# Performance work log

Measured on AMD Instinct MI355X. Metric: run time of the kernel, lower is better.

The kernel has to match this reference:

```python
import jax, jax.numpy as jnp
import numpy as np

N = 240000
B = 2
GRID = (480, 360, 32)
NUM_CLASS = 20
IGNORE_LABEL = 0
MINB = np.array([0.0, -np.pi, -4.0], np.float32)
MAXB = np.array([50.0, np.pi, 2.0], np.float32)
EPS = 1e-5


def setup_inputs() -> dict:
    key = jax.random.key(0)
    ks = jax.random.split(key, 32)
    d = {}
    d['pt_fea'] = jax.random.normal(ks[0], (N, 6), jnp.float32)
    # cylindrical coords (rho, phi, z) uniformly inside the volume
    u = jax.random.uniform(ks[1], (N, 3), jnp.float32)
    d['xyz'] = u * jnp.asarray(MAXB - MINB) + jnp.asarray(MINB)
    d['batch_idx'] = jnp.sort(jax.random.randint(ks[2], (N,), 0, B)).astype(jnp.int64)
    d['pt_lab'] = jax.random.randint(ks[3], (N,), 0, NUM_CLASS).astype(jnp.int64)
    d['shuffled_ind'] = jnp.arange(N, dtype=jnp.int64)  # identity perm (deterministic)
    i = 4
    for name, c in [('bn0', 9), ('bn1', 64), ('bn2', 128), ('bn3', 256)]:
        d[name + '_g'] = jax.random.uniform(ks[i], (c,), jnp.float32, 0.5, 1.5); i += 1
        d[name + '_b'] = jax.random.normal(ks[i], (c,), jnp.float32) * 0.1; i += 1
        d[name + '_m'] = jax.random.normal(ks[i], (c,), jnp.float32) * 0.1; i += 1
        d[name + '_v'] = jax.random.uniform(ks[i], (c,), jnp.float32, 0.5, 1.5); i += 1
    for name, (fi, fo) in [('1', (9, 64)), ('2', (64, 128)), ('3', (128, 256)), ('4', (256, 256))]:
        d['w' + name] = jax.random.normal(ks[i], (fi, fo), jnp.float32) / np.sqrt(fi); i += 1
        d['b' + name] = jax.random.normal(ks[i], (fo,), jnp.float32) * 0.01; i += 1
    d['wc'] = jax.random.normal(ks[i], (256, 16), jnp.float32) / 16.0; i += 1
    d['bc'] = jax.random.normal(ks[i], (16,), jnp.float32) * 0.01
    return d


def _bn(x, g, b, m, v):
    return (x - m) * (g * jax.lax.rsqrt(v + EPS)) + b


def _ppmodel(feat, bn0_g, bn0_b, bn0_m, bn0_v, w1, b1, bn1_g, bn1_b, bn1_m, bn1_v,
             w2, b2, bn2_g, bn2_b, bn2_m, bn2_v, w3, b3, bn3_g, bn3_b, bn3_m, bn3_v, w4, b4):
    x = _bn(feat, bn0_g, bn0_b, bn0_m, bn0_v)
    x = jax.nn.relu(_bn(x @ w1 + b1, bn1_g, bn1_b, bn1_m, bn1_v))
    x = jax.nn.relu(_bn(x @ w2 + b2, bn2_g, bn2_b, bn2_m, bn2_v))
    x = jax.nn.relu(_bn(x @ w3 + b3, bn3_g, bn3_b, bn3_m, bn3_v))
    return x @ w4 + b4  # [N, 256]


def reference(pt_fea, xyz, batch_idx, pt_lab, shuffled_ind,
              bn0_g, bn0_b, bn0_m, bn0_v, w1, b1, bn1_g, bn1_b, bn1_m, bn1_v,
              w2, b2, bn2_g, bn2_b, bn2_m, bn2_v, w3, b3, bn3_g, bn3_b, bn3_m, bn3_v,
              w4, b4, wc, bc):
    minb = jnp.asarray(MINB)
    maxb = jnp.asarray(MAXB)
    grid = jnp.asarray(np.array(GRID, np.float32))
    intervals = (maxb - minb) / (grid - 1.0)

    clamped = jnp.clip(xyz, minb, maxb)
    ind = jnp.floor((clamped - minb) / intervals).astype(jnp.int32)  # [N,3]
    voxel_centers = (ind.astype(jnp.float32) + 0.5) * intervals + minb
    rel_xyz = xyz - voxel_centers
    feat = jnp.concatenate([rel_xyz, pt_fea], axis=1)  # [N,9]

    bi = batch_idx.astype(jnp.int32)
    counts = jnp.full((B,) + GRID + (NUM_CLASS,), IGNORE_LABEL, jnp.int32)
    counts = counts.at[bi, ind[:, 0], ind[:, 1], ind[:, 2], pt_lab].add(1)
    voxel_labels = jnp.argmax(counts, axis=-1).astype(jnp.int32)  # [B,480,360,32]

    feat = feat[shuffled_ind]

    flat = ((bi.astype(jnp.int64) * GRID[0] + ind[:, 0]) * GRID[1] + ind[:, 1]) * GRID[2] + ind[:, 2]
    unq, unq_inv = jnp.unique(flat, size=N, fill_value=-1, return_inverse=True)
    unq_inv = unq_inv.reshape(-1)

    processed = _ppmodel(feat, bn0_g, bn0_b, bn0_m, bn0_v, w1, b1, bn1_g, bn1_b, bn1_m, bn1_v,
                         w2, b2, bn2_g, bn2_b, bn2_m, bn2_v, w3, b3, bn3_g, bn3_b, bn3_m, bn3_v, w4, b4)
    pooled = jax.ops.segment_max(processed, unq_inv, num_segments=N)
    seg_cnt = jax.ops.segment_sum(jnp.ones((N,), jnp.float32), unq_inv, num_segments=N)
    pooled = jnp.where(seg_cnt[:, None] > 0, pooled, 0.0)  # zero out empty (padded) segments

    processed_pooled = jax.nn.relu(pooled @ wc + bc)  # fea_compression

    cat_pt_ind = jnp.concatenate([batch_idx[:, None], ind.astype(jnp.int64)], axis=1)
    return (unq, processed_pooled, voxel_labels, cat_pt_ind)
```

## Files before the change

kernel.cpp:

```cpp
#include <hip/hip_runtime.h>
#include <stdint.h>

#define N_PTS 240000
#define NV    11059200
#define NWORDS 172800
#define NB_PT 938
#define NB_WORD 675
#define NBLK_MLP 3750
#define PA 264

typedef __bf16 bf16x8 __attribute__((ext_vector_type(8)));
typedef short  short8 __attribute__((ext_vector_type(8)));
typedef float  f32x4  __attribute__((ext_vector_type(4)));

__device__ __forceinline__ unsigned short f2bf(float f) {
  unsigned u = __builtin_bit_cast(unsigned, f);
  return (unsigned short)((u + 0x7FFFu + ((u >> 16) & 1u)) >> 16);
}
__device__ __forceinline__ float bf2f(unsigned short h) {
  unsigned u = ((unsigned)h) << 16;
  return __builtin_bit_cast(float, u);
}

__device__ __forceinline__ unsigned block_sum(unsigned v, unsigned* s4, int t) {
  #pragma unroll
  for (int o = 32; o; o >>= 1) v += __shfl_down(v, o);
  if ((t & 63) == 0) s4[t >> 6] = v;
  __syncthreads();
  unsigned r = s4[0] + s4[1] + s4[2] + s4[3];
  __syncthreads();
  return r;
}

__global__ void prep_vox_kernel(
    const float* __restrict__ bng0, const float* __restrict__ bnb0, const float* __restrict__ bnm0, const float* __restrict__ bnv0,
    const float* __restrict__ bng1, const float* __restrict__ bnb1, const float* __restrict__ bnm1, const float* __restrict__ bnv1,
    const float* __restrict__ bng2, const float* __restrict__ bnb2, const float* __restrict__ bnm2, const float* __restrict__ bnv2,
    const float* __restrict__ bng3, const float* __restrict__ bnb3, const float* __restrict__ bnm3, const float* __restrict__ bnv3,
    const float* __restrict__ w1, const float* __restrict__ b1,
    const float* __restrict__ w2, const float* __restrict__ b2,
    const float* __restrict__ w3, const float* __restrict__ b3,
    const float* __restrict__ w4, const float* __restrict__ wc,
    float* __restrict__ s0, float* __restrict__ t0, float* __restrict__ w1e, float* __restrict__ be1,
    float* __restrict__ be2, float* __restrict__ be3,
    unsigned short* __restrict__ w2t, unsigned short* __restrict__ w3t, unsigned short* __restrict__ w4t,
    unsigned short* __restrict__ wct,
    const float* __restrict__ xyz, const int* __restrict__ bidx,
    unsigned* __restrict__ flatkeys, unsigned long long* __restrict__ bitmap,
    float* __restrict__ out_cat, float* __restrict__ out_unq)
{
  if (blockIdx.x < 256) {
    const int id = blockIdx.x * 256 + threadIdx.x;
    { int c = id >> 8, k = id & 255; w4t[c * 256 + k] = f2bf(w4[k * 256 + c]); }
    if (id < 32768) { int c = id >> 7, k = id & 127;
      float s = bng3[c] * rsqrtf(bnv3[c] + 1e-5f);
      w3t[c * 128 + k] = f2bf(w3[k * 256 + c] * s); }
    if (id < 8192) { int c = id >> 6, k = id & 63;
      float s = bng2[c] * rsqrtf(bnv2[c] + 1e-5f);
      w2t[c * 64 + k] = f2bf(w2[k * 128 + c] * s); }
    if (id < 4096) { int c = id >> 8, k = id & 255;
      wct[c * 256 + k] = f2bf(wc[k * 16 + c]); }
    if (id < 576) { int k = id / 64, c = id % 64;
      float s = bng1[c] * rsqrtf(bnv1[c] + 1e-5f);
      w1e[k * 64 + c] = w1[k * 64 + c] * s; }
    if (id < 64)  { float s = bng1[id] * rsqrtf(bnv1[id] + 1e-5f); be1[id] = (b1[id] - bnm1[id]) * s + bnb1[id]; }
    if (id < 128) { float s = bng2[id] * rsqrtf(bnv2[id] + 1e-5f); be2[id] = (b2[id] - bnm2[id]) * s + bnb2[id]; }
    if (id < 256) { float s = bng3[id] * rsqrtf(bnv3[id] + 1e-5f); be3[id] = (b3[id] - bnm3[id]) * s + bnb3[id]; }
    if (id < 9)   { float s = bng0[id] * rsqrtf(bnv0[id] + 1e-5f); s0[id] = s; t0[id] = bnb0[id] - bnm0[id] * s; }
    return;
  }
  const int j = (blockIdx.x - 256) * 256 + threadIdx.x;
  if (j >= N_PTS) return;
  out_unq[j] = -1.0f;
  const float PI_F = 3.14159265358979323846f;
  const float minb[3] = {0.0f, -PI_F, -4.0f};
  const float maxb[3] = {50.0f, PI_F, 2.0f};
  const float gm1[3]  = {479.0f, 359.0f, 31.0f};
  int ind[3];
  #pragma unroll
  for (int d = 0; d < 3; ++d) {
    float itv = (maxb[d] - minb[d]) / gm1[d];
    float x  = xyz[(size_t)j * 3 + d];
    float cl = fminf(fmaxf(x, minb[d]), maxb[d]);
    ind[d] = (int)floorf((cl - minb[d]) / itv);
  }
  const int bi = bidx[j];
  const unsigned flat = ((unsigned)(bi * 480 + ind[0]) * 360u + (unsigned)ind[1]) * 32u + (unsigned)ind[2];
  flatkeys[j] = flat;
  atomicOr(&bitmap[flat >> 6], 1ull << (flat & 63u));
  float* oc = out_cat + (size_t)j * 4;
  oc[0] = (float)bi; oc[1] = (float)ind[0]; oc[2] = (float)ind[1]; oc[3] = (float)ind[2];
}

__global__ void reduce_words(const unsigned long long* __restrict__ bm, unsigned* __restrict__ bsums) {
  __shared__ unsigned sh[256];
  const int w = blockIdx.x * 256 + threadIdx.x;
  sh[threadIdx.x] = (unsigned)__popcll(bm[w]);
  __syncthreads();
  for (int s = 128; s > 0; s >>= 1) { if (threadIdx.x < s) sh[threadIdx.x] += sh[threadIdx.x + s]; __syncthreads(); }
  if (threadIdx.x == 0) bsums[blockIdx.x] = sh[0];
}

__global__ __launch_bounds__(256) void scatter_unq(
    const unsigned long long* __restrict__ bm, const unsigned* __restrict__ bsums,
    unsigned* __restrict__ wordpref, unsigned* __restrict__ unqvals, float* __restrict__ out_unq)
{
  __shared__ unsigned sh[256];
  __shared__ unsigned s4[4];
  const int t = threadIdx.x, b = blockIdx.x;
  const int w = b * 256 + t;
  unsigned long long word = bm[w];
  unsigned own = (unsigned)__popcll(word);
  sh[t] = own; __syncthreads();
  for (int off = 1; off < 256; off <<= 1) {
    unsigned v = (t >= off) ? sh[t - off] : 0u;
    __syncthreads(); sh[t] += v; __syncthreads();
  }
  unsigned v = 0;
  for (int i = t; i < b; i += 256) v += bsums[i];
  const unsigned excl = block_sum(v, s4, t);
  unsigned r = excl + sh[t] - own;
  wordpref[w] = r;
  while (word) {
    int bit = __builtin_ctzll(word);
    unsigned id = (unsigned)w * 64u + (unsigned)bit;
    unqvals[r] = id;
    out_unq[r] = (float)id;
    ++r;
    word &= word - 1;
  }
}

__global__ void inv_kernel(const unsigned* __restrict__ flatkeys, const unsigned long long* __restrict__ bm,
                           const unsigned* __restrict__ wordpref,
                           unsigned* __restrict__ unq_inv, unsigned* __restrict__ cnt) {
  const int j = blockIdx.x * 256 + threadIdx.x;
  if (j >= N_PTS) return;
  const unsigned f = flatkeys[j];
  const unsigned w = f >> 6, b = f & 63u;
  const unsigned r = wordpref[w] + (unsigned)__popcll(bm[w] & ((1ull << b) - 1ull));
  unq_inv[j] = r;
  atomicAdd(&cnt[r], 1u);
}

__global__ void reduce_cnt(const unsigned* __restrict__ cnt, unsigned* __restrict__ bsums) {
  __shared__ unsigned sh[256];
  const int j = blockIdx.x * 256 + threadIdx.x;
  sh[threadIdx.x] = (j < N_PTS) ? cnt[j] : 0u;
  __syncthreads();
  for (int s = 128; s > 0; s >>= 1) { if (threadIdx.x < s) sh[threadIdx.x] += sh[threadIdx.x + s]; __syncthreads(); }
  if (threadIdx.x == 0) bsums[blockIdx.x] = sh[0];
}

__global__ __launch_bounds__(256) void scan_cnt(
    const unsigned* __restrict__ cnt, const unsigned* __restrict__ bsums,
    unsigned* __restrict__ off, unsigned* __restrict__ cur)
{
  __shared__ unsigned sh[256];
  __shared__ unsigned s4[4];
  const int t = threadIdx.x, b = blockIdx.x;
  const int j = b * 256 + t;
  unsigned own = (j < N_PTS) ? cnt[j] : 0u;
  sh[t] = own; __syncthreads();
  for (int o = 1; o < 256; o <<= 1) {
    unsigned v = (t >= o) ? sh[t - o] : 0u;
    __syncthreads(); sh[t] += v; __syncthreads();
  }
  unsigned v = 0;
  for (int i = t; i < b; i += 256) v += bsums[i];
  const unsigned excl = block_sum(v, s4, t);
  if (j < N_PTS) { unsigned e = excl + sh[t] - own; off[j] = e; cur[j] = e; }
}

__global__ void plist_fill_kernel(const unsigned* __restrict__ unq_inv, unsigned* __restrict__ cur,
                                  unsigned long long* __restrict__ plist64,
                                  const unsigned* __restrict__ cnt, const float* __restrict__ bc,
                                  float* __restrict__ out_pooled) {
  const int j = blockIdx.x * 256 + threadIdx.x;
  if (j >= N_PTS) return;
  const unsigned r = unq_inv[j];
  plist64[atomicAdd(&cur[r], 1u)] = ((unsigned long long)r << 32) | (unsigned)j;
  if (cnt[j] == 0) {
    #pragma unroll
    for (int c = 0; c < 16; ++c) out_pooled[(size_t)j * 16 + c] = fmaxf(bc[c], 0.f);
  }
}

template<int K, int C, bool RELU, bool MIDB>
__device__ __forceinline__ void gemm_stage(
    const unsigned short* __restrict__ Wt,
    const float* __restrict__ bias,
    const unsigned short* in,
    unsigned short* outp,
    int wave, int l15, int quad)
{
  constexpr int KC = K / 32;
  constexpr int NT = C / 128;
  f32x4 acc[4][NT];
  #pragma unroll
  for (int mt = 0; mt < 4; ++mt)
    #pragma unroll
    for (int nt = 0; nt < NT; ++nt) acc[mt][nt] = (f32x4){0.f, 0.f, 0.f, 0.f};
  const unsigned short* wp[NT];
  #pragma unroll
  for (int nt = 0; nt < NT; ++nt)
    wp[nt] = Wt + (size_t)(wave * 16 * NT + nt * 16 + l15) * K + quad * 8;
  #pragma unroll
  for (int kc = 0; kc < KC; ++kc) {
    bf16x8 b[NT];
    #pragma unroll
    for (int nt = 0; nt < NT; ++nt)
      b[nt] = __builtin_bit_cast(bf16x8, *(const short8*)(wp[nt] + kc * 32));
    #pragma unroll
    for (int mt = 0; mt < 4; ++mt) {
      bf16x8 a = __builtin_bit_cast(bf16x8, *(const short8*)&in[(mt * 16 + l15) * PA + kc * 32 + quad * 8]);
      #pragma unroll
      for (int nt = 0; nt < NT; ++nt)
        acc[mt][nt] = __builtin_amdgcn_mfma_f32_16x16x32_bf16(b[nt], a, acc[mt][nt], 0, 0, 0);
    }
  }
  if (MIDB) __syncthreads();
  #pragma unroll
  for (int mt = 0; mt < 4; ++mt)
    #pragma unroll
    for (int nt = 0; nt < NT; ++nt) {
      const int cbase = wave * 16 * NT + nt * 16 + quad * 4;
      const f32x4 bs = *(const f32x4*)&bias[cbase];
      unsigned short h[4];
      #pragma unroll
      for (int r = 0; r < 4; ++r) {
        float y = acc[mt][nt][r] + bs[r];
        if (RELU) y = fmaxf(y, 0.f);
        h[r] = f2bf(y);
      }
      uint2 pk; pk.x = (unsigned)h[0] | ((unsigned)h[1] << 16);
      pk.y = (unsigned)h[2] | ((unsigned)h[3] << 16);
      *(uint2*)&outp[(mt * 16 + l15) * PA + cbase] = pk;
    }
  __syncthreads();
}

__global__ __launch_bounds__(512, 8) void mlp_pool_kernel(
    const float* __restrict__ ptfea, const float* __restrict__ xyz, const int* __restrict__ shuf,
    const unsigned long long* __restrict__ plist64,
    const unsigned* __restrict__ offv, const unsigned* __restrict__ cnt,
    const int* __restrict__ ptlab, const unsigned* __restrict__ unqvals,
    const float* __restrict__ s0, const float* __restrict__ t0,
    const float* __restrict__ w1e, const float* __restrict__ be1,
    const unsigned short* __restrict__ w2t, const float* __restrict__ be2,
    const unsigned short* __restrict__ w3t, const float* __restrict__ be3,
    const unsigned short* __restrict__ w4t, const float* __restrict__ b4,
    const unsigned short* __restrict__ wct, const float* __restrict__ bc,
    unsigned short* __restrict__ partials, float* __restrict__ out_pooled,
    float* __restrict__ out_lab)
{
  __shared__ __align__(16) unsigned short buf[64 * PA];
  __shared__ int segs[64];
  __shared__ int jrows[64];
  __shared__ int s_alast;
  __shared__ int s_nrun;
  __shared__ unsigned short s_runs[32];
  __shared__ unsigned char s_lead[64], s_comp[64];
  const int tid  = threadIdx.x;
  const int wave = tid >> 6, lane = tid & 63;
  const int l15 = lane & 15, quad = lane >> 4;
  const int row0 = blockIdx.x * 64;

  if (tid == 0) { s_alast = 0; s_nrun = 0; }
  if (tid < 64) {
    const unsigned long long v = plist64[row0 + tid];
    jrows[tid] = (int)(unsigned)v;
    segs[tid]  = (int)(unsigned)(v >> 32);
  }

  {
    const int r = tid >> 3, part = tid & 7;
    const int sj = shuf[(unsigned)plist64[row0 + r]];
    const float PI_F = 3.14159265358979323846f;
    const float minb[3] = {0.0f, -PI_F, -4.0f};
    const float maxb[3] = {50.0f, PI_F, 2.0f};
    const float gm1[3]  = {479.0f, 359.0f, 31.0f};
    float x0[9];
    #pragma unroll
    for (int d = 0; d < 3; ++d) {
      float itv = (maxb[d] - minb[d]) / gm1[d];
      float x   = xyz[(size_t)sj * 3 + d];
      float cl  = fminf(fmaxf(x, minb[d]), maxb[d]);
      float fi  = floorf((cl - minb[d]) / itv);
      float center = (fi + 0.5f) * itv + minb[d];
      x0[d] = (x - center) * s0[d] + t0[d];
    }
    #pragma unroll
    for (int d = 0; d < 6; ++d) x0[3 + d] = ptfea[(size_t)sj * 6 + d] * s0[3 + d] + t0[3 + d];
    unsigned short h[8];
    #pragma unroll
    for (int ci = 0; ci < 8; ++ci) {
      float acc = be1[part * 8 + ci];
      #pragma unroll
      for (int k = 0; k < 9; ++k) acc += x0[k] * w1e[k * 64 + part * 8 + ci];
      h[ci] = f2bf(fmaxf(acc, 0.0f));
    }
    *(short8*)&buf[r * PA + part * 8] = *(short8*)&h[0];
  }
  __syncthreads();

  if (tid < 64) {
    const int r = tid;
    bool lead = (r == 0) || (segs[r] != segs[r - 1]);
    s_lead[r] = lead ? 1 : 0;
    unsigned char comp = 0;
    int e = r + 1;
    if (lead) {
      atomicMax(&s_alast, r);
      while (e < 64 && segs[e] == segs[r]) ++e;
      const unsigned s = (unsigned)segs[r];
      comp = (offv[s] == (unsigned)(row0 + r) && offv[s] + cnt[s] == (unsigned)(row0 + e)) ? 1 : 0;
    }
    s_comp[r] = comp;
    if (comp) {
      int bestl;
      if (e - r == 1) bestl = ptlab[jrows[r]];
      else {
        int bestc = 0; bestl = 32;
        for (int i = r; i < e; ++i) {
          const int li = ptlab[jrows[i]];
          int cc = 0;
          for (int k2 = r; k2 < e; ++k2) cc += (ptlab[jrows[k2]] == li) ? 1 : 0;
          if (cc > bestc || (cc == bestc && li < bestl)) { bestc = cc; bestl = li; }
        }
      }
      out_lab[unqvals[segs[r]]] = (float)bestl;
    }
    const bool multi = lead && (e - r) > 1;
    unsigned long long mm = __ballot(multi);
    if (multi) {
      int idx = (int)__popcll(mm & ((1ull << r) - 1ull));
      s_runs[idx] = (unsigned short)((r << 8) | e);
    }
    if (tid == 0) s_nrun = (int)__popcll(mm);
  }

  gemm_stage< 64, 128, true,  false>(w2t, be2, buf,       buf + 136, wave, l15, quad);
  gemm_stage<128, 256, true,  true >(w3t, be3, buf + 136, buf,       wave, l15, quad);
  gemm_stage<256, 256, false, true >(w4t, b4,  buf,       buf,       wave, l15, quad);

  if (tid < 256) {
    const int n = s_nrun;
    for (int i = 0; i < n; ++i) {
      const int re = s_runs[i];
      const int r = re >> 8, e = re & 255;
      float m = bf2f(buf[r * PA + tid]);
      for (int rr = r + 1; rr < e; ++rr) m = fmaxf(m, bf2f(buf[rr * PA + tid]));
      buf[r * PA + tid] = f2bf(m);
    }
  }
  __syncthreads();

  if (tid < 256) {
    const int c = tid;
    const int alast = s_alast;
    const size_t b2 = (size_t)blockIdx.x * 2;
    if (!s_comp[0])     partials[b2 * 256 + c]       = buf[0 * PA + c];
    if (!s_comp[alast]) partials[(b2 + 1) * 256 + c] = buf[alast * PA + c];
  }

  if (wave < 4) {
    const unsigned short* wp = wct + l15 * 256 + quad * 8;
    f32x4 acc = (f32x4){0.f, 0.f, 0.f, 0.f};
    #pragma unroll
    for (int kc = 0; kc < 8; ++kc) {
      bf16x8 w = __builtin_bit_cast(bf16x8, *(const short8*)(wp + kc * 32));
      bf16x8 x = __builtin_bit_cast(bf16x8, *(const short8*)&buf[(wave * 16 + l15) * PA + kc * 32 + quad * 8]);
      acc = __builtin_amdgcn_mfma_f32_16x16x32_bf16(w, x, acc, 0, 0, 0);
    }
    const int r1 = wave * 16 + l15;
    if (s_lead[r1] && s_comp[r1]) {
      const f32x4 bcv = *(const f32x4*)&bc[quad * 4];
      f32x4 v;
      #pragma unroll
      for (int r = 0; r < 4; ++r) v[r] = fmaxf(acc[r] + bcv[r], 0.f);
      *(f32x4*)&out_pooled[(size_t)segs[r1] * 16 + quad * 4] = v;
    }
  }
}

__global__ __launch_bounds__(256) void merge_kernel(
    const unsigned long long* __restrict__ plist64,
    const unsigned* __restrict__ offv, const unsigned* __restrict__ cnt,
    const unsigned short* __restrict__ partials,
    const int* __restrict__ ptlab, const unsigned* __restrict__ unqvals,
    const float* __restrict__ wc, const float* __restrict__ bc,
    float* __restrict__ out_pooled, float* __restrict__ out_lab)
{
  __shared__ float pooled[256];
  __shared__ float psum[256];
  const int b = blockIdx.x;
  const unsigned s = (unsigned)(plist64[(size_t)b * 64 + 63] >> 32);
  const unsigned o = offv[s], e = o + cnt[s];
  if ((o >> 6) != (unsigned)b) return;
  if (e <= (unsigned)(b + 1) * 64) return;
  const int B1 = (int)((e - 1) >> 6);
  const int c = threadIdx.x;
  float m = bf2f(partials[((size_t)2 * b + 1) * 256 + c]);
  for (int bb = b + 1; bb <= B1; ++bb)
    m = fmaxf(m, bf2f(partials[(size_t)2 * bb * 256 + c]));
  pooled[c] = m;
  __syncthreads();
  const int co = c & 15, kg = c >> 4;
  float p = 0.f;
  #pragma unroll
  for (int k = kg * 16; k < kg * 16 + 16; ++k) p += pooled[k] * wc[k * 16 + co];
  psum[c] = p;
  __syncthreads();
  if (c < 16) {
    float acc = bc[c];
    #pragma unroll
    for (int g = 0; g < 16; ++g) acc += psum[g * 16 + c];
    out_pooled[(size_t)s * 16 + c] = fmaxf(acc, 0.f);
  }
  if (c == 0) {
    int bestc = 0, bestl = 32;
    for (unsigned i = o; i < e; ++i) {
      const int li = ptlab[(unsigned)plist64[i]];
      int cc = 0;
      for (unsigned k2 = o; k2 < e; ++k2) cc += (ptlab[(unsigned)plist64[k2]] == li) ? 1 : 0;
      if (cc > bestc || (cc == bestc && li < bestl)) { bestc = cc; bestl = li; }
    }
    out_lab[unqvals[s]] = (float)bestl;
  }
}

extern "C" void kernel_launch(void* const* d_in, const int* in_sizes, int n_in,
                              void* d_out, int out_size, void* d_ws, size_t ws_size,
                              hipStream_t stream)
{
  const float* pt_fea = (const float*)d_in[0];
  const float* xyz    = (const float*)d_in[1];
  const int*   bidx   = (const int*)d_in[2];
  const int*   ptlab  = (const int*)d_in[3];
  const int*   shuf   = (const int*)d_in[4];
  const float* bng0 = (const float*)d_in[5],  *bnb0 = (const float*)d_in[6],  *bnm0 = (const float*)d_in[7],  *bnv0 = (const float*)d_in[8];
  const float* bng1 = (const float*)d_in[9],  *bnb1 = (const float*)d_in[10], *bnm1 = (const float*)d_in[11], *bnv1 = (const float*)d_in[12];
  const float* bng2 = (const float*)d_in[13], *bnb2 = (const float*)d_in[14], *bnm2 = (const float*)d_in[15], *bnv2 = (const float*)d_in[16];
  const float* bng3 = (const float*)d_in[17], *bnb3 = (const float*)d_in[18], *bnm3 = (const float*)d_in[19], *bnv3 = (const float*)d_in[20];
  const float* w1 = (const float*)d_in[21], *b1 = (const float*)d_in[22];
  const float* w2 = (const float*)d_in[23], *b2 = (const float*)d_in[24];
  const float* w3 = (const float*)d_in[25], *b3 = (const float*)d_in[26];
  const float* w4 = (const float*)d_in[27], *b4 = (const float*)d_in[28];
  const float* wc = (const float*)d_in[29], *bc = (const float*)d_in[30];

  float* out        = (float*)d_out;
  float* out_unq    = out;
  float* out_pooled = out + 240000;
  float* out_lab    = out + 4080000;
  float* out_cat    = out + 15139200;

  char* wsb = (char*)d_ws;
  size_t o = 0;
  auto alloc = [&](size_t bytes) -> void* { void* p = wsb + o; o = (o + bytes + 255) & ~(size_t)255; return p; };
  unsigned long long* bitmap = (unsigned long long*)alloc((size_t)NWORDS * 8);
  unsigned* cnt    = (unsigned*)alloc((size_t)N_PTS * 4);
  const size_t zero_bytes = o;
  float* s0  = (float*)alloc(9 * 4);
  float* t0  = (float*)alloc(9 * 4);
  float* w1e = (float*)alloc(576 * 4);
  float* be1 = (float*)alloc(64 * 4);
  float* be2 = (float*)alloc(128 * 4);
  float* be3 = (float*)alloc(256 * 4);
  unsigned short* w2t = (unsigned short*)alloc(8192 * 2);
  unsigned short* w3t = (unsigned short*)alloc(32768 * 2);
  unsigned short* w4t = (unsigned short*)alloc(65536 * 2);
  unsigned short* wct = (unsigned short*)alloc(4096 * 2);
  unsigned* flatkeys = (unsigned*)alloc((size_t)N_PTS * 4);
  unsigned* unq_inv  = (unsigned*)alloc((size_t)N_PTS * 4);
  unsigned* unqvals  = (unsigned*)alloc((size_t)N_PTS * 4);
  unsigned* offv     = (unsigned*)alloc((size_t)N_PTS * 4);
  unsigned* cur      = (unsigned*)alloc((size_t)N_PTS * 4);
  unsigned long long* plist64 = (unsigned long long*)alloc((size_t)N_PTS * 8);
  unsigned* wordpref = (unsigned*)alloc((size_t)NWORDS * 4);
  unsigned* bsumA    = (unsigned*)alloc(NB_WORD * 4);
  unsigned* bsumB    = (unsigned*)alloc(NB_PT * 4);
  unsigned short* partials = (unsigned short*)alloc((size_t)NBLK_MLP * 2 * 256 * 2);

  hipMemsetAsync(bitmap, 0, zero_bytes, stream);
  hipMemsetAsync(out_lab, 0, (size_t)NV * 4, stream);

  prep_vox_kernel<<<256 + NB_PT, 256, 0, stream>>>(
      bng0, bnb0, bnm0, bnv0, bng1, bnb1, bnm1, bnv1,
      bng2, bnb2, bnm2, bnv2, bng3, bnb3, bnm3, bnv3,
      w1, b1, w2, b2, w3, b3, w4, wc,
      s0, t0, w1e, be1, be2, be3, w2t, w3t, w4t, wct,
      xyz, bidx, flatkeys, bitmap, out_cat, out_unq);
  reduce_words<<<NB_WORD, 256, 0, stream>>>(bitmap, bsumA);
  scatter_unq<<<NB_WORD, 256, 0, stream>>>(bitmap, bsumA, wordpref, unqvals, out_unq);
  inv_kernel<<<NB_PT, 256, 0, stream>>>(flatkeys, bitmap, wordpref, unq_inv, cnt);
  reduce_cnt<<<NB_PT, 256, 0, stream>>>(cnt, bsumB);
  scan_cnt<<<NB_PT, 256, 0, stream>>>(cnt, bsumB, offv, cur);
  plist_fill_kernel<<<NB_PT, 256, 0, stream>>>(unq_inv, cur, plist64, cnt, bc, out_pooled);
  mlp_pool_kernel<<<NBLK_MLP, 512, 0, stream>>>(pt_fea, xyz, shuf, plist64, offv, cnt,
                                                ptlab, unqvals,
                                                s0, t0, w1e, be1, w2t, be2, w3t, be3, w4t, b4,
                                                wct, bc, partials, out_pooled, out_lab);
  merge_kernel<<<NBLK_MLP, 256, 0, stream>>>(plist64, offv, cnt, partials,
                                             ptlab, unqvals, wc, bc, out_pooled, out_lab);
}
```

Baseline: 402.4 us.

## Process two 64-row windows per block to reuse weight fragments; fuse zeroing into prep

The MLP/pool kernel now runs 256-thread blocks that each handle two 64-point windows. Every wave loads a weight fragment once and applies it to both windows' activations, so global weight traffic per point is halved. The cost is twice the LDS per block and more accumulator registers (launch bounds 256,2), which lowers occupancy. The separate memset of the label volume and of cnt is also folded into the prep kernel as a grid-stride zeroing loop, removing one memset launch.

```diff
diff --git a/kernel.cpp b/kernel.cpp
--- a/kernel.cpp
+++ b/kernel.cpp
@@ -6,7 +6,8 @@
 #define NWORDS 172800
 #define NB_PT 938
 #define NB_WORD 675
-#define NBLK_MLP 3750
+#define NWIN   3750
+#define NBLK_MLP 1875
 #define PA 264
 
 typedef __bf16 bf16x8 __attribute__((ext_vector_type(8)));
@@ -47,10 +48,15 @@
     unsigned short* __restrict__ wct,
     const float* __restrict__ xyz, const int* __restrict__ bidx,
     unsigned* __restrict__ flatkeys, unsigned long long* __restrict__ bitmap,
-    float* __restrict__ out_cat, float* __restrict__ out_unq)
-{
+    unsigned* __restrict__ cnt,
+    float* __restrict__ out_cat, float* __restrict__ out_unq, float* __restrict__ out_lab)
+{
+  const int gtid = blockIdx.x * 256 + threadIdx.x;
+  for (unsigned i = (unsigned)gtid; i < NV / 4; i += (256 + NB_PT) * 256)
+    *(f32x4*)&out_lab[(size_t)i * 4] = (f32x4){0.f, 0.f, 0.f, 0.f};
+  if (gtid < N_PTS) cnt[gtid] = 0u;
   if (blockIdx.x < 256) {
-    const int id = blockIdx.x * 256 + threadIdx.x;
+    const int id = gtid;
     { int c = id >> 8, k = id & 255; w4t[c * 256 + k] = f2bf(w4[k * 256 + c]); }
     if (id < 32768) { int c = id >> 7, k = id & 127;
       float s = bng3[c] * rsqrtf(bnv3[c] + 1e-5f);
@@ -187,20 +193,20 @@
 }
 
 template<int K, int C, bool RELU, bool MIDB>
-__device__ __forceinline__ void gemm_stage(
+__device__ __forceinline__ void gemm_stage2(
     const unsigned short* __restrict__ Wt,
     const float* __restrict__ bias,
-    const unsigned short* in,
-    unsigned short* outp,
+    const unsigned short* inA, unsigned short* outA,
+    const unsigned short* inB, unsigned short* outB,
     int wave, int l15, int quad)
 {
   constexpr int KC = K / 32;
-  constexpr int NT = C / 128;
-  f32x4 acc[4][NT];
+  constexpr int NT = C / 64;
+  f32x4 accA[4][NT], accB[4][NT];
   #pragma unroll
   for (int mt = 0; mt < 4; ++mt)
     #pragma unroll
-    for (int nt = 0; nt < NT; ++nt) acc[mt][nt] = (f32x4){0.f, 0.f, 0.f, 0.f};
+    for (int nt = 0; nt < NT; ++nt) { accA[mt][nt] = (f32x4){0.f,0.f,0.f,0.f}; accB[mt][nt] = (f32x4){0.f,0.f,0.f,0.f}; }
   const unsigned short* wp[NT];
   #pragma unroll
   for (int nt = 0; nt < NT; ++nt)
@@ -213,10 +219,13 @@
       b[nt] = __builtin_bit_cast(bf16x8, *(const short8*)(wp[nt] + kc * 32));
     #pragma unroll
     for (int mt = 0; mt < 4; ++mt) {
-      bf16x8 a = __builtin_bit_cast(bf16x8, *(const short8*)&in[(mt * 16 + l15) * PA + kc * 32 + quad * 8]);
+      bf16x8 aA = __builtin_bit_cast(bf16x8, *(const short8*)&inA[(mt * 16 + l15) * PA + kc * 32 + quad * 8]);
+      bf16x8 aB = __builtin_bit_cast(bf16x8, *(const short8*)&inB[(mt * 16 + l15) * PA + kc * 32 + quad * 8]);
       #pragma unroll
-      for (int nt = 0; nt < NT; ++nt)
-        acc[mt][nt] = __builtin_amdgcn_mfma_f32_16x16x32_bf16(b[nt], a, acc[mt][nt], 0, 0, 0);
+      for (int nt = 0; nt < NT; ++nt) {
+        accA[mt][nt] = __builtin_amdgcn_mfma_f32_16x16x32_bf16(b[nt], aA, accA[mt][nt], 0, 0, 0);
+        accB[mt][nt] = __builtin_amdgcn_mfma_f32_16x16x32_bf16(b[nt], aB, accB[mt][nt], 0, 0, 0);
+      }
     }
   }
   if (MIDB) __syncthreads();
@@ -226,21 +235,23 @@
     for (int nt = 0; nt < NT; ++nt) {
       const int cbase = wave * 16 * NT + nt * 16 + quad * 4;
       const f32x4 bs = *(const f32x4*)&bias[cbase];
-      unsigned short h[4];
+      unsigned short hA[4], hB[4];
       #pragma unroll
       for (int r = 0; r < 4; ++r) {
-        float y = acc[mt][nt][r] + bs[r];
-        if (RELU) y = fmaxf(y, 0.f);
-        h[r] = f2bf(y);
+        float yA = accA[mt][nt][r] + bs[r];
+        float yB = accB[mt][nt][r] + bs[r];
+        if (RELU) { yA = fmaxf(yA, 0.f); yB = fmaxf(yB, 0.f); }
+        hA[r] = f2bf(yA); hB[r] = f2bf(yB);
       }
-      uint2 pk; pk.x = (unsigned)h[0] | ((unsigned)h[1] << 16);
-      pk.y = (unsigned)h[2] | ((unsigned)h[3] << 16);
-      *(uint2*)&outp[(mt * 16 + l15) * PA + cbase] = pk;
-    }
-  __syncthreads();
-}
-
-__global__ __launch_bounds__(512, 8) void mlp_pool_kernel(
+      uint2 pkA; pkA.x = (unsigned)hA[0] | ((unsigned)hA[1] << 16); pkA.y = (unsigned)hA[2] | ((unsigned)hA[3] << 16);
+      uint2 pkB; pkB.x = (unsigned)hB[0] | ((unsigned)hB[1] << 16); pkB.y = (unsigned)hB[2] | ((unsigned)hB[3] << 16);
+      *(uint2*)&outA[(mt * 16 + l15) * PA + cbase] = pkA;
+      *(uint2*)&outB[(mt * 16 + l15) * PA + cbase] = pkB;
+    }
+  __syncthreads();
+}
+
+__global__ __launch_bounds__(256, 2) void mlp_pool_kernel(
     const float* __restrict__ ptfea, const float* __restrict__ xyz, const int* __restrict__ shuf,
     const unsigned long long* __restrict__ plist64,
     const unsigned* __restrict__ offv, const unsigned* __restrict__ cnt,
@@ -254,28 +265,31 @@
     unsigned short* __restrict__ partials, float* __restrict__ out_pooled,
     float* __restrict__ out_lab)
 {
-  __shared__ __align__(16) unsigned short buf[64 * PA];
-  __shared__ int segs[64];
-  __shared__ int jrows[64];
-  __shared__ int s_alast;
-  __shared__ int s_nrun;
-  __shared__ unsigned short s_runs[32];
-  __shared__ unsigned char s_lead[64], s_comp[64];
+  __shared__ __align__(16) unsigned short bufA[64 * PA];
+  __shared__ __align__(16) unsigned short bufB[64 * PA];
+  __shared__ int segs[128];
+  __shared__ int jrows[128];
+  __shared__ int s_alast[2];
+  __shared__ int s_nrun[2];
+  __shared__ unsigned short s_runs[2][32];
+  __shared__ unsigned char s_lead[128], s_comp[128];
   const int tid  = threadIdx.x;
   const int wave = tid >> 6, lane = tid & 63;
   const int l15 = lane & 15, quad = lane >> 4;
-  const int row0 = blockIdx.x * 64;
-
-  if (tid == 0) { s_alast = 0; s_nrun = 0; }
-  if (tid < 64) {
-    const unsigned long long v = plist64[row0 + tid];
+  const int rowbase = blockIdx.x * 128;
+
+  if (tid < 2) { s_alast[tid] = 0; s_nrun[tid] = 0; }
+  if (tid < 128) {
+    const unsigned long long v = plist64[rowbase + tid];
     jrows[tid] = (int)(unsigned)v;
     segs[tid]  = (int)(unsigned)(v >> 32);
   }
 
-  {
-    const int r = tid >> 3, part = tid & 7;
-    const int sj = shuf[(unsigned)plist64[row0 + r]];
+  #pragma unroll
+  for (int w = 0; w < 2; ++w) {
+    const int rl = tid >> 2, part = tid & 3;
+    const int sj = shuf[(unsigned)plist64[rowbase + w * 64 + rl]];
+    unsigned short* bf = w ? bufB : bufA;
     const float PI_F = 3.14159265358979323846f;
     const float minb[3] = {0.0f, -PI_F, -4.0f};
     const float maxb[3] = {50.0f, PI_F, 2.0f};
@@ -292,94 +306,102 @@
     }
     #pragma unroll
     for (int d = 0; d < 6; ++d) x0[3 + d] = ptfea[(size_t)sj * 6 + d] * s0[3 + d] + t0[3 + d];
-    unsigned short h[8];
-    #pragma unroll
-    for (int ci = 0; ci < 8; ++ci) {
-      float acc = be1[part * 8 + ci];
+    unsigned short h[16];
+    #pragma unroll
+    for (int ci = 0; ci < 16; ++ci) {
+      float acc = be1[part * 16 + ci];
       #pragma unroll
-      for (int k = 0; k < 9; ++k) acc += x0[k] * w1e[k * 64 + part * 8 + ci];
+      for (int k = 0; k < 9; ++k) acc += x0[k] * w1e[k * 64 + part * 16 + ci];
       h[ci] = f2bf(fmaxf(acc, 0.0f));
     }
-    *(short8*)&buf[r * PA + part * 8] = *(short8*)&h[0];
-  }
-  __syncthreads();
-
-  if (tid < 64) {
-    const int r = tid;
-    bool lead = (r == 0) || (segs[r] != segs[r - 1]);
-    s_lead[r] = lead ? 1 : 0;
+    *(short8*)&bf[rl * PA + part * 16]     = *(short8*)&h[0];
+    *(short8*)&bf[rl * PA + part * 16 + 8] = *(short8*)&h[8];
+  }
+  __syncthreads();
+
+  if (tid < 128) {
+    const int w = tid >> 6, rl = tid & 63;
+    const int wbase = w * 64;
+    bool lead = (rl == 0) || (segs[tid] != segs[tid - 1]);
+    s_lead[tid] = lead ? 1 : 0;
     unsigned char comp = 0;
-    int e = r + 1;
+    int e = rl + 1;
     if (lead) {
-      atomicMax(&s_alast, r);
-      while (e < 64 && segs[e] == segs[r]) ++e;
-      const unsigned s = (unsigned)segs[r];
-      comp = (offv[s] == (unsigned)(row0 + r) && offv[s] + cnt[s] == (unsigned)(row0 + e)) ? 1 : 0;
-    }
-    s_comp[r] = comp;
+      atomicMax(&s_alast[w], rl);
+      while (e < 64 && segs[wbase + e] == segs[tid]) ++e;
+      const unsigned s = (unsigned)segs[tid];
+      comp = (offv[s] == (unsigned)(rowbase + wbase + rl) &&
+              offv[s] + cnt[s] == (unsigned)(rowbase + wbase + e)) ? 1 : 0;
+    }
+    s_comp[tid] = comp;
     if (comp) {
       int bestl;
-      if (e - r == 1) bestl = ptlab[jrows[r]];
+      if (e - rl == 1) bestl = ptlab[jrows[tid]];
       else {
         int bestc = 0; bestl = 32;
-        for (int i = r; i < e; ++i) {
-          const int li = ptlab[jrows[i]];
+        for (int i = rl; i < e; ++i) {
+          const int li = ptlab[jrows[wbase + i]];
           int cc = 0;
-          for (int k2 = r; k2 < e; ++k2) cc += (ptlab[jrows[k2]] == li) ? 1 : 0;
+          for (int k2 = rl; k2 < e; ++k2) cc += (ptlab[jrows[wbase + k2]] == li) ? 1 : 0;
           if (cc > bestc || (cc == bestc && li < bestl)) { bestc = cc; bestl = li; }
         }
       }
-      out_lab[unqvals[segs[r]]] = (float)bestl;
-    }
-    const bool multi = lead && (e - r) > 1;
+      out_lab[unqvals[segs[tid]]] = (float)bestl;
+    }
+    const bool multi = lead && (e - rl) > 1;
     unsigned long long mm = __ballot(multi);
     if (multi) {
-      int idx = (int)__popcll(mm & ((1ull << r) - 1ull));
-      s_runs[idx] = (unsigned short)((r << 8) | e);
-    }
-    if (tid == 0) s_nrun = (int)__popcll(mm);
-  }
-
-  gemm_stage< 64, 128, true,  false>(w2t, be2, buf,       buf + 136, wave, l15, quad);
-  gemm_stage<128, 256, true,  true >(w3t, be3, buf + 136, buf,       wave, l15, quad);
-  gemm_stage<256, 256, false, true >(w4t, b4,  buf,       buf,       wave, l15, quad);
-
-  if (tid < 256) {
-    const int n = s_nrun;
+      int idx = (int)__popcll(mm & ((1ull << rl) - 1ull));
+      s_runs[w][idx] = (unsigned short)((rl << 8) | e);
+    }
+    if (rl == 0) s_nrun[w] = (int)__popcll(mm);
+  }
+
+  gemm_stage2< 64, 128, true,  false>(w2t, be2, bufA,       bufA + 136, bufB,       bufB + 136, wave, l15, quad);
+  gemm_stage2<128, 256, true,  true >(w3t, be3, bufA + 136, bufA,       bufB + 136, bufB,       wave, l15, quad);
+  gemm_stage2<256, 256, false, true >(w4t, b4,  bufA,       bufA,       bufB,       bufB,       wave, l15, quad);
+
+  #pragma unroll
+  for (int w = 0; w < 2; ++w) {
+    unsigned short* bf = w ? bufB : bufA;
+    const int n = s_nrun[w];
     for (int i = 0; i < n; ++i) {
-      const int re = s_runs[i];
+      const int re = s_runs[w][i];
       const int r = re >> 8, e = re & 255;
-      float m = bf2f(buf[r * PA + tid]);
-      for (int rr = r + 1; rr < e; ++rr) m = fmaxf(m, bf2f(buf[rr * PA + tid]));
-      buf[r * PA + tid] = f2bf(m);
-    }
-  }
-  __syncthreads();
-
-  if (tid < 256) {
-    const int c = tid;
-    const int alast = s_alast;
-    const size_t b2 = (size_t)blockIdx.x * 2;
-    if (!s_comp[0])     partials[b2 * 256 + c]       = buf[0 * PA + c];
-    if (!s_comp[alast]) partials[(b2 + 1) * 256 + c] = buf[alast * PA + c];
-  }
-
-  if (wave < 4) {
+      float m = bf2f(bf[r * PA + tid]);
+      for (int rr = r + 1; rr < e; ++rr) m = fmaxf(m, bf2f(bf[rr * PA + tid]));
+      bf[r * PA + tid] = f2bf(m);
+    }
+  }
+  __syncthreads();
+
+  #pragma unroll
+  for (int w = 0; w < 2; ++w) {
+    const unsigned short* bf = w ? bufB : bufA;
+    const int alast = s_alast[w];
+    const size_t b2 = ((size_t)blockIdx.x * 2 + w) * 2;
+    if (!s_comp[w * 64])         partials[b2 * 256 + tid]       = bf[0 * PA + tid];
+    if (!s_comp[w * 64 + alast]) partials[(b2 + 1) * 256 + tid] = bf[alast * PA + tid];
+  }
+
+  #pragma unroll
+  for (int w = 0; w < 2; ++w) {
+    const unsigned short* bf = w ? bufB : bufA;
     const unsigned short* wp = wct + l15 * 256 + quad * 8;
     f32x4 acc = (f32x4){0.f, 0.f, 0.f, 0.f};
     #pragma unroll
     for (int kc = 0; kc < 8; ++kc) {
-      bf16x8 w = __builtin_bit_cast(bf16x8, *(const short8*)(wp + kc * 32));
-      bf16x8 x = __builtin_bit_cast(bf16x8, *(const short8*)&buf[(wave * 16 + l15) * PA + kc * 32 + quad * 8]);
-      acc = __builtin_amdgcn_mfma_f32_16x16x32_bf16(w, x, acc, 0, 0, 0);
-    }
-    const int r1 = wave * 16 + l15;
-    if (s_lead[r1] && s_comp[r1]) {
+      bf16x8 wv = __builtin_bit_cast(bf16x8, *(const short8*)(wp + kc * 32));
+      bf16x8 x  = __builtin_bit_cast(bf16x8, *(const short8*)&bf[(wave * 16 + l15) * PA + kc * 32 + quad * 8]);
+      acc = __builtin_amdgcn_mfma_f32_16x16x32_bf16(wv, x, acc, 0, 0, 0);
+    }
+    const int g = w * 64 + wave * 16 + l15;
+    if (s_lead[g] && s_comp[g]) {
       const f32x4 bcv = *(const f32x4*)&bc[quad * 4];
       f32x4 v;
       #pragma unroll
       for (int r = 0; r < 4; ++r) v[r] = fmaxf(acc[r] + bcv[r], 0.f);
-      *(f32x4*)&out_pooled[(size_t)segs[r1] * 16 + quad * 4] = v;
+      *(f32x4*)&out_pooled[(size_t)segs[g] * 16 + quad * 4] = v;
     }
   }
 }
@@ -459,8 +481,8 @@
   size_t o = 0;
   auto alloc = [&](size_t bytes) -> void* { void* p = wsb + o; o = (o + bytes + 255) & ~(size_t)255; return p; };
   unsigned long long* bitmap = (unsigned long long*)alloc((size_t)NWORDS * 8);
+  const size_t zero_bytes = o;
   unsigned* cnt    = (unsigned*)alloc((size_t)N_PTS * 4);
-  const size_t zero_bytes = o;
   float* s0  = (float*)alloc(9 * 4);
   float* t0  = (float*)alloc(9 * 4);
   float* w1e = (float*)alloc(576 * 4);
@@ -480,27 +502,26 @@
   unsigned* wordpref = (unsigned*)alloc((size_t)NWORDS * 4);
   unsigned* bsumA    = (unsigned*)alloc(NB_WORD * 4);
   unsigned* bsumB    = (unsigned*)alloc(NB_PT * 4);
-  unsigned short* partials = (unsigned short*)alloc((size_t)NBLK_MLP * 2 * 256 * 2);
+  unsigned short* partials = (unsigned short*)alloc((size_t)NWIN * 2 * 256 * 2);
 
   hipMemsetAsync(bitmap, 0, zero_bytes, stream);
-  hipMemsetAsync(out_lab, 0, (size_t)NV * 4, stream);
 
   prep_vox_kernel<<<256 + NB_PT, 256, 0, stream>>>(
       bng0, bnb0, bnm0, bnv0, bng1, bnb1, bnm1, bnv1,
       bng2, bnb2, bnm2, bnv2, bng3, bnb3, bnm3, bnv3,
       w1, b1, w2, b2, w3, b3, w4, wc,
       s0, t0, w1e, be1, be2, be3, w2t, w3t, w4t, wct,
-      xyz, bidx, flatkeys, bitmap, out_cat, out_unq);
+      xyz, bidx, flatkeys, bitmap, cnt, out_cat, out_unq, out_lab);
   reduce_words<<<NB_WORD, 256, 0, stream>>>(bitmap, bsumA);
   scatter_unq<<<NB_WORD, 256, 0, stream>>>(bitmap, bsumA, wordpref, unqvals, out_unq);
   inv_kernel<<<NB_PT, 256, 0, stream>>>(flatkeys, bitmap, wordpref, unq_inv, cnt);
   reduce_cnt<<<NB_PT, 256, 0, stream>>>(cnt, bsumB);
   scan_cnt<<<NB_PT, 256, 0, stream>>>(cnt, bsumB, offv, cur);
   plist_fill_kernel<<<NB_PT, 256, 0, stream>>>(unq_inv, cur, plist64, cnt, bc, out_pooled);
-  mlp_pool_kernel<<<NBLK_MLP, 512, 0, stream>>>(pt_fea, xyz, shuf, plist64, offv, cnt,
+  mlp_pool_kernel<<<NBLK_MLP, 256, 0, stream>>>(pt_fea, xyz, shuf, plist64, offv, cnt,
                                                 ptlab, unqvals,
                                                 s0, t0, w1e, be1, w2t, be2, w3t, be3, w4t, b4,
                                                 wct, bc, partials, out_pooled, out_lab);
-  merge_kernel<<<NBLK_MLP, 256, 0, stream>>>(plist64, offv, cnt, partials,
-                                             ptlab, unqvals, wc, bc, out_pooled, out_lab);
-}
+  merge_kernel<<<NWIN, 256, 0, stream>>>(plist64, offv, cnt, partials,
+                                         ptlab, unqvals, wc, bc, out_pooled, out_lab);
+}
```

Result: faster. 393.5 us (-2.2%).
